# Optimization experiments

Measured on AMD Instinct MI355X. Metric: run time of the kernel, lower is better.

The kernel has to match this reference:

```python
import jax, jax.numpy as jnp
import numpy as np

B, N, C, H = 2, 2048, 1024, 16
HD = C // H
FF = 2 * C


def _layernorm(x, w, b, eps=1e-5):
    mu = jnp.mean(x, axis=-1, keepdims=True)
    var = jnp.var(x, axis=-1, keepdims=True)
    return (x - mu) * jax.lax.rsqrt(var + eps) * w + b


def setup_inputs() -> dict:
    key = jax.random.key(0)
    ks = jax.random.split(key, 16)
    std = 0.02
    d = {
        'q': jax.random.normal(ks[0], (B, N, C), jnp.float32),
        'k': jax.random.normal(ks[1], (B, N, C), jnp.float32),
        'v': jax.random.normal(ks[2], (B, N, C), jnp.float32),
        # attention projections (stored [in, out])
        'Wq': jax.random.normal(ks[3], (C, C), jnp.float32) * std,
        'bq': jnp.zeros((C,), jnp.float32),
        'Wk': jax.random.normal(ks[4], (C, C), jnp.float32) * std,
        'bk': jnp.zeros((C,), jnp.float32),
        'Wv': jax.random.normal(ks[5], (C, C), jnp.float32) * std,
        'bv': jnp.zeros((C,), jnp.float32),
        'Wo': jax.random.normal(ks[6], (C, C), jnp.float32) * std,
        'bo': jnp.zeros((C,), jnp.float32),
        # post-attention LayerNorm
        'ln_w': jnp.ones((C,), jnp.float32),
        'ln_b': jnp.zeros((C,), jnp.float32),
        # FFN
        'W1': jax.random.normal(ks[7], (C, FF), jnp.float32) * std,
        'b1': jnp.zeros((FF,), jnp.float32),
        'W2': jax.random.normal(ks[8], (FF, C), jnp.float32) * std,
        'b2': jnp.zeros((C,), jnp.float32),
    }
    return d


def reference(q, k, v, Wq, bq, Wk, bk, Wv, bv, Wo, bo, ln_w, ln_b, W1, b1, W2, b2):
    scale = HD ** -0.5
    # Note: the torch forward overwrites the normalized-input attention with
    # attention on raw q,k,v; only the second call affects the output.
    qh = (q @ Wq + bq).reshape(B, N, H, HD)  # [B,Nq,H,hd]
    kh = (k @ Wk + bk).reshape(B, N, H, HD)
    vh = (v @ Wv + bv).reshape(B, N, H, HD)
    attn = jnp.einsum('bqhd,bkhd->bhqk', qh, kh) * scale
    attn = jax.nn.softmax(attn, axis=-1)
    ctx = jnp.einsum('bhqk,bkhd->bqhd', attn, vh).reshape(B, N, C)
    x = ctx @ Wo + bo
    x = x + q  # residual (drop_path=0, dropout eval -> identity)
    h = _layernorm(x, ln_w, ln_b)
    y = jax.nn.gelu(h @ W1 + b1, approximate=False) @ W2 + b2
    return y + x
```

## Files before the change

kernel.cpp:

```cpp
#include <hip/hip_runtime.h>

constexpr int B_ = 2, N_ = 2048, C_ = 1024, H_ = 16, HD_ = 64, FF_ = 2048;

typedef __attribute__((ext_vector_type(8))) __bf16 bf16x8;
typedef __attribute__((ext_vector_type(4))) float f32x4;
typedef __attribute__((ext_vector_type(4))) short s16x4;

__device__ __forceinline__ unsigned short f2bf(float f) {
  union { float f; unsigned int u; } v; v.f = f;
  unsigned int r = v.u + 0x7fffu + ((v.u >> 16) & 1u);
  return (unsigned short)(r >> 16);
}

__device__ __forceinline__ void gload_lds16(const unsigned short* g, unsigned short* l) {
  __builtin_amdgcn_global_load_lds((const __attribute__((address_space(1))) void*)g,
                                   (__attribute__((address_space(3))) void*)l, 16, 0, 0);
}

__global__ __launch_bounds__(256)
void cast3_bf16(const float* __restrict__ q, const float* __restrict__ k,
                const float* __restrict__ v, unsigned short* __restrict__ qo,
                unsigned short* __restrict__ ko, unsigned short* __restrict__ vo, int n8) {
  int i = blockIdx.x * 256 + threadIdx.x;
  if (i >= n8) return;
  const float* in = blockIdx.z == 0 ? q : (blockIdx.z == 1 ? k : v);
  unsigned short* out = blockIdx.z == 0 ? qo : (blockIdx.z == 1 ? ko : vo);
  const float4 a = ((const float4*)in)[2 * i];
  const float4 b = ((const float4*)in)[2 * i + 1];
  uint4 o;
  o.x = (unsigned)f2bf(a.x) | ((unsigned)f2bf(a.y) << 16);
  o.y = (unsigned)f2bf(a.z) | ((unsigned)f2bf(a.w) << 16);
  o.z = (unsigned)f2bf(b.x) | ((unsigned)f2bf(b.y) << 16);
  o.w = (unsigned)f2bf(b.z) | ((unsigned)f2bf(b.w) << 16);
  ((uint4*)out)[i] = o;
}

__global__ __launch_bounds__(256)
void wt_cast(const float* __restrict__ W, unsigned short* __restrict__ Wt, int K, int N) {
  __shared__ unsigned short tile[32][33];
  const int tx = threadIdx.x, ty = threadIdx.y;
  const int n0 = blockIdx.x * 32, k0 = blockIdx.y * 32;
#pragma unroll
  for (int r = 0; r < 4; ++r)
    tile[ty + r * 8][tx] = f2bf(W[(size_t)(k0 + ty + r * 8) * N + n0 + tx]);
  __syncthreads();
#pragma unroll
  for (int r = 0; r < 4; ++r)
    Wt[(size_t)(n0 + ty + r * 8) * K + k0 + tx] = tile[tx][ty + r * 8];
}

__global__ __launch_bounds__(256)
void wt_cast4(const float* __restrict__ Wa, const float* __restrict__ Wb,
              const float* __restrict__ Wc, const float* __restrict__ Wd,
              unsigned short* __restrict__ Oa, unsigned short* __restrict__ Ob,
              unsigned short* __restrict__ Oc, unsigned short* __restrict__ Od) {
  __shared__ unsigned short tile[32][33];
  const int z = blockIdx.z;
  const float* W = z == 0 ? Wa : (z == 1 ? Wb : (z == 2 ? Wc : Wd));
  unsigned short* Wt = z == 0 ? Oa : (z == 1 ? Ob : (z == 2 ? Oc : Od));
  const int tx = threadIdx.x, ty = threadIdx.y;
  const int n0 = blockIdx.x * 32, k0 = blockIdx.y * 32;
#pragma unroll
  for (int r = 0; r < 4; ++r)
    tile[ty + r * 8][tx] = f2bf(W[(size_t)(k0 + ty + r * 8) * C_ + n0 + tx]);
  __syncthreads();
#pragma unroll
  for (int r = 0; r < 4; ++r)
    Wt[(size_t)(n0 + ty + r * 8) * C_ + k0 + tx] = tile[tx][ty + r * 8];
}

__global__ __launch_bounds__(256)
void vh_transpose(const unsigned short* __restrict__ Vh, unsigned short* __restrict__ VhT) {
  __shared__ unsigned short tile[32][33];
  const int tx = threadIdx.x, ty = threadIdx.y;
  const int bh = blockIdx.z, b = bh >> 4, h = bh & 15;
  const int n0 = blockIdx.x * 32, d0 = blockIdx.y * 32;
#pragma unroll
  for (int r = 0; r < 4; ++r) {
    int n = n0 + ty + r * 8;
    tile[ty + r * 8][tx] = Vh[((size_t)(b * N_ + n)) * C_ + h * HD_ + d0 + tx];
  }
  __syncthreads();
#pragma unroll
  for (int r = 0; r < 4; ++r) {
    int d = d0 + ty + r * 8;
    VhT[((size_t)(bh * HD_ + d)) * N_ + n0 + tx] = tile[tx][ty + r * 8];
  }
}

__global__ __launch_bounds__(256, 2)
void gemm_qkv(const unsigned short* __restrict__ A0, const unsigned short* __restrict__ A1,
              const unsigned short* __restrict__ A2, const unsigned short* __restrict__ B0,
              const unsigned short* __restrict__ B1, const unsigned short* __restrict__ B2,
              const float* __restrict__ c0, const float* __restrict__ c1v,
              const float* __restrict__ c2, unsigned short* __restrict__ O0,
              unsigned short* __restrict__ O1, unsigned short* __restrict__ O2) {
  const int z = blockIdx.z;
  const unsigned short* A = z == 0 ? A0 : (z == 1 ? A1 : A2);
  const unsigned short* Bt = z == 0 ? B0 : (z == 1 ? B1 : B2);
  const float* bias = z == 0 ? c0 : (z == 1 ? c1v : c2);
  unsigned short* outB = z == 0 ? O0 : (z == 1 ? O1 : O2);
  const int K = C_, Nn = C_;

  __shared__ unsigned short lA[128 * 64];
  __shared__ unsigned short lB[128 * 64];
  const int t = threadIdx.x;
  const int lane = t & 63;
  const int w = t >> 6;
  const int wm = w >> 1, wn = w & 1;
  const int l15 = lane & 15, g = lane >> 4;

  const unsigned short* Ab = A + (size_t)blockIdx.x * 128 * K;
  const unsigned short* Bb = Bt + (size_t)blockIdx.y * 128 * K;

  f32x4 acc[4][4] = {};

  for (int k0 = 0; k0 < K; k0 += 64) {
    __syncthreads();
#pragma unroll
    for (int i = 0; i < 4; ++i) {
      int id = i * 256 + t;
      gload_lds16(Ab + (size_t)(id >> 3) * K + k0 + (id & 7) * 8, &lA[id * 8]);
    }
#pragma unroll
    for (int i = 0; i < 4; ++i) {
      int id = i * 256 + t;
      gload_lds16(Bb + (size_t)(id >> 3) * K + k0 + (id & 7) * 8, &lB[id * 8]);
    }
    __syncthreads();
#pragma unroll
    for (int kk = 0; kk < 2; ++kk) {
      bf16x8 af[4], bfr[4];
#pragma unroll
      for (int mi = 0; mi < 4; ++mi)
        af[mi] = *(const bf16x8*)&lA[(wm * 64 + mi * 16 + l15) * 64 + kk * 32 + g * 8];
#pragma unroll
      for (int ni = 0; ni < 4; ++ni)
        bfr[ni] = *(const bf16x8*)&lB[(wn * 64 + ni * 16 + l15) * 64 + kk * 32 + g * 8];
#pragma unroll
      for (int mi = 0; mi < 4; ++mi)
#pragma unroll
        for (int ni = 0; ni < 4; ++ni)
          acc[mi][ni] = __builtin_amdgcn_mfma_f32_16x16x32_bf16(af[mi], bfr[ni], acc[mi][ni], 0, 0, 0);
    }
  }

#pragma unroll
  for (int mi = 0; mi < 4; ++mi)
#pragma unroll
    for (int ni = 0; ni < 4; ++ni) {
      const int col = blockIdx.y * 128 + wn * 64 + ni * 16 + l15;
      const float bcol = bias[col];
#pragma unroll
      for (int r = 0; r < 4; ++r) {
        const int row = blockIdx.x * 128 + wm * 64 + mi * 16 + g * 4 + r;
        outB[(size_t)row * Nn + col] = f2bf(acc[mi][ni][r] + bcol);
      }
    }
}

template <int EPI>
__global__ __launch_bounds__(256, 2)
void gemm_bt(const unsigned short* __restrict__ A, const unsigned short* __restrict__ Bt,
             const float* __restrict__ bias, const float* __restrict__ resid,
             float* __restrict__ outF, unsigned short* __restrict__ outB,
             int M, int N, int K) {
  __shared__ unsigned short lA[128 * 64];
  __shared__ unsigned short lB[128 * 64];
  const int t = threadIdx.x;
  const int lane = t & 63;
  const int w = t >> 6;
  const int wm = w >> 1, wn = w & 1;
  const int l15 = lane & 15, g = lane >> 4;

  const unsigned short* Ab = A + (size_t)blockIdx.x * 128 * K;
  const unsigned short* Bb = Bt + (size_t)blockIdx.y * 128 * K;

  f32x4 acc[4][4] = {};

  for (int k0 = 0; k0 < K; k0 += 64) {
    __syncthreads();
#pragma unroll
    for (int i = 0; i < 4; ++i) {
      int id = i * 256 + t;
      gload_lds16(Ab + (size_t)(id >> 3) * K + k0 + (id & 7) * 8, &lA[id * 8]);
    }
#pragma unroll
    for (int i = 0; i < 4; ++i) {
      int id = i * 256 + t;
      gload_lds16(Bb + (size_t)(id >> 3) * K + k0 + (id & 7) * 8, &lB[id * 8]);
    }
    __syncthreads();
#pragma unroll
    for (int kk = 0; kk < 2; ++kk) {
      bf16x8 af[4], bfr[4];
#pragma unroll
      for (int mi = 0; mi < 4; ++mi)
        af[mi] = *(const bf16x8*)&lA[(wm * 64 + mi * 16 + l15) * 64 + kk * 32 + g * 8];
#pragma unroll
      for (int ni = 0; ni < 4; ++ni)
        bfr[ni] = *(const bf16x8*)&lB[(wn * 64 + ni * 16 + l15) * 64 + kk * 32 + g * 8];
#pragma unroll
      for (int mi = 0; mi < 4; ++mi)
#pragma unroll
        for (int ni = 0; ni < 4; ++ni)
          acc[mi][ni] = __builtin_amdgcn_mfma_f32_16x16x32_bf16(af[mi], bfr[ni], acc[mi][ni], 0, 0, 0);
    }
  }

#pragma unroll
  for (int mi = 0; mi < 4; ++mi)
#pragma unroll
    for (int ni = 0; ni < 4; ++ni) {
      const int col = blockIdx.y * 128 + wn * 64 + ni * 16 + l15;
      const float bcol = bias[col];
#pragma unroll
      for (int r = 0; r < 4; ++r) {
        const int row = blockIdx.x * 128 + wm * 64 + mi * 16 + g * 4 + r;
        const size_t o = (size_t)row * N + col;
        float val = acc[mi][ni][r] + bcol;
        if (EPI == 0) {
          outB[o] = f2bf(val);
        } else if (EPI == 1) {
          outF[o] = val + resid[o];
        } else {
          float ge = 0.5f * val * (1.0f + erff(val * 0.70710678118654752f));
          outB[o] = f2bf(ge);
        }
      }
    }
}

__global__ __launch_bounds__(256, 2)
void gemm_n64(const unsigned short* __restrict__ A, const unsigned short* __restrict__ Bt,
              const float* __restrict__ bias, const float* __restrict__ resid,
              float* __restrict__ outF, int M, int N, int K) {
  __shared__ unsigned short lA[128 * 64];
  __shared__ unsigned short lB[64 * 64];
  const int t = threadIdx.x;
  const int lane = t & 63;
  const int w = t >> 6;
  const int wm = w >> 1, wn = w & 1;
  const int l15 = lane & 15, g = lane >> 4;

  const unsigned short* Ab = A + (size_t)blockIdx.x * 128 * K;
  const unsigned short* Bb = Bt + (size_t)blockIdx.y * 64 * K;

  f32x4 acc[4][2] = {};

  for (int k0 = 0; k0 < K; k0 += 64) {
    __syncthreads();
#pragma unroll
    for (int i = 0; i < 4; ++i) {
      int id = i * 256 + t;
      gload_lds16(Ab + (size_t)(id >> 3) * K + k0 + (id & 7) * 8, &lA[id * 8]);
    }
#pragma unroll
    for (int i = 0; i < 2; ++i) {
      int id = i * 256 + t;
      gload_lds16(Bb + (size_t)(id >> 3) * K + k0 + (id & 7) * 8, &lB[id * 8]);
    }
    __syncthreads();
#pragma unroll
    for (int kk = 0; kk < 2; ++kk) {
      bf16x8 af[4], bfr[2];
#pragma unroll
      for (int mi = 0; mi < 4; ++mi)
        af[mi] = *(const bf16x8*)&lA[(wm * 64 + mi * 16 + l15) * 64 + kk * 32 + g * 8];
#pragma unroll
      for (int ni = 0; ni < 2; ++ni)
        bfr[ni] = *(const bf16x8*)&lB[(wn * 32 + ni * 16 + l15) * 64 + kk * 32 + g * 8];
#pragma unroll
      for (int mi = 0; mi < 4; ++mi)
#pragma unroll
        for (int ni = 0; ni < 2; ++ni)
          acc[mi][ni] = __builtin_amdgcn_mfma_f32_16x16x32_bf16(af[mi], bfr[ni], acc[mi][ni], 0, 0, 0);
    }
  }

#pragma unroll
  for (int mi = 0; mi < 4; ++mi)
#pragma unroll
    for (int ni = 0; ni < 2; ++ni) {
      const int col = blockIdx.y * 64 + wn * 32 + ni * 16 + l15;
      const float bcol = bias[col];
#pragma unroll
      for (int r = 0; r < 4; ++r) {
        const int row = blockIdx.x * 128 + wm * 64 + mi * 16 + g * 4 + r;
        const size_t o = (size_t)row * N + col;
        outF[o] = acc[mi][ni][r] + bcol + resid[o];
      }
    }
}

__global__ __launch_bounds__(256, 2)
void attn_fwd(const unsigned short* __restrict__ Qh, const unsigned short* __restrict__ Kh,
              const unsigned short* __restrict__ VhT, unsigned short* __restrict__ ctx) {
  __shared__ unsigned short lK[2][64 * 64];
  __shared__ unsigned short lV[2][64 * 64];

  const int t = threadIdx.x, lane = t & 63, w = t >> 6;
  const int l15 = lane & 15, g = lane >> 4;
  const int bh = blockIdx.y, b = bh >> 4, h = bh & 15;
  const int qb0 = blockIdx.x * 128 + w * 32;

  const unsigned short* Qb = Qh + (size_t)b * N_ * C_ + h * HD_;
  const unsigned short* Kb = Kh + (size_t)b * N_ * C_ + h * HD_;
  const unsigned short* Vb = VhT + (size_t)bh * HD_ * N_;

  bf16x8 qf[2][2];
#pragma unroll
  for (int qi = 0; qi < 2; ++qi)
#pragma unroll
    for (int kk = 0; kk < 2; ++kk)
      qf[qi][kk] = *(const bf16x8*)(Qb + (size_t)(qb0 + qi * 16 + l15) * C_ + kk * 32 + g * 8);

  auto stageK = [&](int buf, int kb) {
#pragma unroll
    for (int i = 0; i < 2; ++i) {
      int o = (i * 256 + t) * 16;
      int r = o >> 7;
      int c = (o & 127) ^ ((r & 7) << 4);
      gload_lds16(Kb + (size_t)(kb + r) * C_ + (c >> 1), &lK[buf][o >> 1]);
    }
  };
  auto stageV = [&](int buf, int kb) {
#pragma unroll
    for (int i = 0; i < 2; ++i) {
      int o = (i * 256 + t) * 16;
      int r = o >> 7;
      int c = (o & 127) ^ ((r & 7) << 4);
      gload_lds16(Vb + (size_t)r * N_ + kb + (c >> 1), &lV[buf][o >> 1]);
    }
  };

  f32x4 od[4][2] = {};
  float mrun[2] = {-1e30f, -1e30f};
  float srun[2] = {0.f, 0.f};
  const float c1 = 0.18033688011112042f;
  const float DTHR = 8.0f / 0.18033688011112042f;

  stageK(0, 0);
  stageV(0, 0);
  __syncthreads();

  int cur = 0;
  for (int tile = 0; tile < N_ / 64; ++tile) {
    if (tile + 1 < N_ / 64) {
      stageK(cur ^ 1, (tile + 1) * 64);
      stageV(cur ^ 1, (tile + 1) * 64);
    }

    f32x4 st[4][2];
#pragma unroll
    for (int kf = 0; kf < 4; ++kf) {
      const int krow = kf * 16 + l15;
      const int sw = (krow & 7) << 4;
      const bf16x8 ka = *(const bf16x8*)&lK[cur][krow * 64 + ((( g * 16) ^ sw) >> 1)];
      const bf16x8 kc = *(const bf16x8*)&lK[cur][krow * 64 + (((64 + g * 16) ^ sw) >> 1)];
#pragma unroll
      for (int qi = 0; qi < 2; ++qi) {
        f32x4 z = {};
        z = __builtin_amdgcn_mfma_f32_16x16x32_bf16(ka, qf[qi][0], z, 0, 0, 0);
        z = __builtin_amdgcn_mfma_f32_16x16x32_bf16(kc, qf[qi][1], z, 0, 0, 0);
        st[kf][qi] = z;
      }
    }

    s16x4 pb[4][2];
#pragma unroll
    for (int qi = 0; qi < 2; ++qi) {
      float mx = st[0][qi][0];
#pragma unroll
      for (int r = 1; r < 4; ++r) mx = fmaxf(mx, st[0][qi][r]);
#pragma unroll
      for (int kf = 1; kf < 4; ++kf)
#pragma unroll
        for (int r = 0; r < 4; ++r) mx = fmaxf(mx, st[kf][qi][r]);
      mx = fmaxf(mx, __shfl_xor(mx, 16));
      mx = fmaxf(mx, __shfl_xor(mx, 32));
      if (__any(mx > mrun[qi] + DTHR)) {
        const float mn = fmaxf(mrun[qi], mx);
        const float sf = exp2f((mrun[qi] - mn) * c1);
        mrun[qi] = mn;
        srun[qi] *= sf;
#pragma unroll
        for (int di = 0; di < 4; ++di)
#pragma unroll
          for (int r = 0; r < 4; ++r) od[di][qi][r] *= sf;
      }
      const float mc = mrun[qi] * c1;
#pragma unroll
      for (int kf = 0; kf < 4; ++kf) {
        union { s16x4 v; __bf16 e[4]; } u;
#pragma unroll
        for (int r = 0; r < 4; ++r) {
          float pv = exp2f(st[kf][qi][r] * c1 - mc);
          srun[qi] += pv;
          u.e[r] = (__bf16)pv;
        }
        pb[kf][qi] = u.v;
      }
    }

#pragma unroll
    for (int di = 0; di < 4; ++di) {
      const int vrow = di * 16 + l15;
      const int sw = (vrow & 7) << 4;
#pragma unroll
      for (int kf = 0; kf < 4; ++kf) {
        const s16x4 vt = *(const s16x4*)&lV[cur][vrow * 64 + (((kf * 32 + g * 8) ^ sw) >> 1)];
#pragma unroll
        for (int qi = 0; qi < 2; ++qi)
          od[di][qi] = __builtin_amdgcn_mfma_f32_16x16x16bf16_1k(vt, pb[kf][qi], od[di][qi], 0, 0, 0);
      }
    }

    __syncthreads();
    cur ^= 1;
  }

#pragma unroll
  for (int qi = 0; qi < 2; ++qi) {
    float s = srun[qi];
    s += __shfl_xor(s, 16);
    s += __shfl_xor(s, 32);
    float rinv = 1.0f / s;
    const int q = qb0 + qi * 16 + l15;
#pragma unroll
    for (int di = 0; di < 4; ++di)
#pragma unroll
      for (int r = 0; r < 4; ++r) {
        int d = di * 16 + g * 4 + r;
        ctx[((size_t)(b * N_ + q)) * C_ + h * HD_ + d] = f2bf(od[di][qi][r] * rinv);
      }
  }
}

__global__ __launch_bounds__(256)
void ln_kernel(const float* __restrict__ x, const float* __restrict__ lw,
               const float* __restrict__ lb, unsigned short* __restrict__ h) {
  const int row = blockIdx.x;
  const int t = threadIdx.x;
  const float4 v = ((const float4*)(x + (size_t)row * C_))[t];
  float sum = v.x + v.y + v.z + v.w;
#pragma unroll
  for (int m = 1; m < 64; m <<= 1) sum += __shfl_xor(sum, m);
  __shared__ float red[8];
  if ((t & 63) == 0) red[t >> 6] = sum;
  __syncthreads();
  const float mu = (red[0] + red[1] + red[2] + red[3]) * (1.0f / C_);
  const float d0 = v.x - mu, d1 = v.y - mu, d2 = v.z - mu, d3 = v.w - mu;
  float sq = d0 * d0 + d1 * d1 + d2 * d2 + d3 * d3;
#pragma unroll
  for (int m = 1; m < 64; m <<= 1) sq += __shfl_xor(sq, m);
  if ((t & 63) == 0) red[4 + (t >> 6)] = sq;
  __syncthreads();
  const float var = (red[4] + red[5] + red[6] + red[7]) * (1.0f / C_);
  const float rstd = rsqrtf(var + 1e-5f);
  const float4 ww = ((const float4*)lw)[t];
  const float4 bb = ((const float4*)lb)[t];
  uint2 o;
  o.x = (unsigned)f2bf(d0 * rstd * ww.x + bb.x) | ((unsigned)f2bf(d1 * rstd * ww.y + bb.y) << 16);
  o.y = (unsigned)f2bf(d2 * rstd * ww.z + bb.z) | ((unsigned)f2bf(d3 * rstd * ww.w + bb.w) << 16);
  ((uint2*)(h + (size_t)row * C_))[t] = o;
}

extern "C" void kernel_launch(void* const* d_in, const int* in_sizes, int n_in,
                              void* d_out, int out_size, void* d_ws, size_t ws_size,
                              hipStream_t stream) {
  const float* q   = (const float*)d_in[0];
  const float* k   = (const float*)d_in[1];
  const float* v   = (const float*)d_in[2];
  const float* Wq  = (const float*)d_in[3];
  const float* bq  = (const float*)d_in[4];
  const float* Wk  = (const float*)d_in[5];
  const float* bk  = (const float*)d_in[6];
  const float* Wv  = (const float*)d_in[7];
  const float* bv  = (const float*)d_in[8];
  const float* Wo  = (const float*)d_in[9];
  const float* bo  = (const float*)d_in[10];
  const float* lnw = (const float*)d_in[11];
  const float* lnb = (const float*)d_in[12];
  const float* W1  = (const float*)d_in[13];
  const float* b1  = (const float*)d_in[14];
  const float* W2  = (const float*)d_in[15];
  const float* b2  = (const float*)d_in[16];
  float* out = (float*)d_out;

  char* ws = (char*)d_ws;
  const size_t MB = 1024 * 1024;
  if (ws_size < 120 * MB) return;
  unsigned short* qb   = (unsigned short*)(ws + 0 * MB);
  unsigned short* kb   = (unsigned short*)(ws + 8 * MB);
  unsigned short* vb   = (unsigned short*)(ws + 16 * MB);
  unsigned short* Wqt  = (unsigned short*)(ws + 24 * MB);
  unsigned short* Wkt  = (unsigned short*)(ws + 26 * MB);
  unsigned short* Wvt  = (unsigned short*)(ws + 28 * MB);
  unsigned short* Wot  = (unsigned short*)(ws + 30 * MB);
  unsigned short* W1t  = (unsigned short*)(ws + 32 * MB);
  unsigned short* W2t  = (unsigned short*)(ws + 36 * MB);
  unsigned short* Qh   = (unsigned short*)(ws + 40 * MB);
  unsigned short* Kh   = (unsigned short*)(ws + 48 * MB);
  unsigned short* Vh   = (unsigned short*)(ws + 56 * MB);
  unsigned short* VhT  = (unsigned short*)(ws + 64 * MB);
  unsigned short* ctx  = (unsigned short*)(ws + 72 * MB);
  float*          xf   = (float*)(ws + 80 * MB);
  unsigned short* hb   = (unsigned short*)(ws + 96 * MB);
  unsigned short* tbuf = (unsigned short*)(ws + 104 * MB);

  const int n8 = B_ * N_ * C_ / 8;
  cast3_bf16<<<dim3((n8 + 255) / 256, 1, 3), 256, 0, stream>>>(q, k, v, qb, kb, vb, n8);

  dim3 blk32(32, 8);
  wt_cast4<<<dim3(C_ / 32, C_ / 32, 4), blk32, 0, stream>>>(Wq, Wk, Wv, Wo, Wqt, Wkt, Wvt, Wot);
  wt_cast<<<dim3(FF_ / 32, C_ / 32), blk32, 0, stream>>>(W1, W1t, C_, FF_);
  wt_cast<<<dim3(C_ / 32, FF_ / 32), blk32, 0, stream>>>(W2, W2t, FF_, C_);

  gemm_qkv<<<dim3(B_ * N_ / 128, C_ / 128, 3), 256, 0, stream>>>(qb, kb, vb, Wqt, Wkt, Wvt,
                                                                 bq, bk, bv, Qh, Kh, Vh);

  vh_transpose<<<dim3(N_ / 32, HD_ / 32, B_ * H_), blk32, 0, stream>>>(Vh, VhT);
  attn_fwd<<<dim3(N_ / 128, B_ * H_), 256, 0, stream>>>(Qh, Kh, VhT, ctx);

  gemm_n64<<<dim3(B_ * N_ / 128, C_ / 64), 256, 0, stream>>>(ctx, Wot, bo, q, xf, B_ * N_, C_, C_);
  ln_kernel<<<dim3(B_ * N_), 256, 0, stream>>>(xf, lnw, lnb, hb);
  gemm_bt<2><<<dim3(B_ * N_ / 128, FF_ / 128), 256, 0, stream>>>(hb, W1t, b1, nullptr, nullptr, tbuf,
                                                                 B_ * N_, FF_, C_);
  gemm_n64<<<dim3(B_ * N_ / 128, C_ / 64), 256, 0, stream>>>(tbuf, W2t, b2, xf, out, B_ * N_, C_, FF_);
}
```

Baseline: 245.3 us.

## Split attention block into 8 waves of 16 queries with MFMA priority hints

The attention kernel now launches 512 threads per block, so each of 8 waves handles 16 query rows instead of 4 waves handling 32. This halves per-wave register state (accumulators, scores, softmax stats), and each thread issues one staging load per tile instead of two. The change also raises occupancy bounds, wraps MFMA sections in s_setprio, and packs the output stores into 8-byte writes. In exchange, each wave reuses a K/V tile fragment across fewer queries, adding LDS read traffic per MFMA, and more waves wait at each barrier.

```diff
diff --git a/kernel.cpp b/kernel.cpp
--- a/kernel.cpp
+++ b/kernel.cpp
@@ -293,7 +293,7 @@
     }
 }
 
-__global__ __launch_bounds__(256, 2)
+__global__ __launch_bounds__(512, 4)
 void attn_fwd(const unsigned short* __restrict__ Qh, const unsigned short* __restrict__ Kh,
               const unsigned short* __restrict__ VhT, unsigned short* __restrict__ ctx) {
   __shared__ unsigned short lK[2][64 * 64];
@@ -302,41 +302,33 @@
   const int t = threadIdx.x, lane = t & 63, w = t >> 6;
   const int l15 = lane & 15, g = lane >> 4;
   const int bh = blockIdx.y, b = bh >> 4, h = bh & 15;
-  const int qb0 = blockIdx.x * 128 + w * 32;
+  const int qb0 = blockIdx.x * 128 + w * 16;
 
   const unsigned short* Qb = Qh + (size_t)b * N_ * C_ + h * HD_;
   const unsigned short* Kb = Kh + (size_t)b * N_ * C_ + h * HD_;
   const unsigned short* Vb = VhT + (size_t)bh * HD_ * N_;
 
-  bf16x8 qf[2][2];
-#pragma unroll
-  for (int qi = 0; qi < 2; ++qi)
-#pragma unroll
-    for (int kk = 0; kk < 2; ++kk)
-      qf[qi][kk] = *(const bf16x8*)(Qb + (size_t)(qb0 + qi * 16 + l15) * C_ + kk * 32 + g * 8);
+  bf16x8 qf[2];
+#pragma unroll
+  for (int kk = 0; kk < 2; ++kk)
+    qf[kk] = *(const bf16x8*)(Qb + (size_t)(qb0 + l15) * C_ + kk * 32 + g * 8);
 
   auto stageK = [&](int buf, int kb) {
-#pragma unroll
-    for (int i = 0; i < 2; ++i) {
-      int o = (i * 256 + t) * 16;
-      int r = o >> 7;
-      int c = (o & 127) ^ ((r & 7) << 4);
-      gload_lds16(Kb + (size_t)(kb + r) * C_ + (c >> 1), &lK[buf][o >> 1]);
-    }
+    int o = t * 16;
+    int r = o >> 7;
+    int c = (o & 127) ^ ((r & 7) << 4);
+    gload_lds16(Kb + (size_t)(kb + r) * C_ + (c >> 1), &lK[buf][o >> 1]);
   };
   auto stageV = [&](int buf, int kb) {
-#pragma unroll
-    for (int i = 0; i < 2; ++i) {
-      int o = (i * 256 + t) * 16;
-      int r = o >> 7;
-      int c = (o & 127) ^ ((r & 7) << 4);
-      gload_lds16(Vb + (size_t)r * N_ + kb + (c >> 1), &lV[buf][o >> 1]);
-    }
+    int o = t * 16;
+    int r = o >> 7;
+    int c = (o & 127) ^ ((r & 7) << 4);
+    gload_lds16(Vb + (size_t)r * N_ + kb + (c >> 1), &lV[buf][o >> 1]);
   };
 
-  f32x4 od[4][2] = {};
-  float mrun[2] = {-1e30f, -1e30f};
-  float srun[2] = {0.f, 0.f};
+  f32x4 od[4] = {};
+  float mrun = -1e30f;
+  float srun = 0.f;
   const float c1 = 0.18033688011112042f;
   const float DTHR = 8.0f / 0.18033688011112042f;
 
@@ -351,58 +343,55 @@
       stageV(cur ^ 1, (tile + 1) * 64);
     }
 
-    f32x4 st[4][2];
+    f32x4 st[4];
+    __builtin_amdgcn_s_setprio(1);
 #pragma unroll
     for (int kf = 0; kf < 4; ++kf) {
       const int krow = kf * 16 + l15;
       const int sw = (krow & 7) << 4;
       const bf16x8 ka = *(const bf16x8*)&lK[cur][krow * 64 + ((( g * 16) ^ sw) >> 1)];
       const bf16x8 kc = *(const bf16x8*)&lK[cur][krow * 64 + (((64 + g * 16) ^ sw) >> 1)];
-#pragma unroll
-      for (int qi = 0; qi < 2; ++qi) {
-        f32x4 z = {};
-        z = __builtin_amdgcn_mfma_f32_16x16x32_bf16(ka, qf[qi][0], z, 0, 0, 0);
-        z = __builtin_amdgcn_mfma_f32_16x16x32_bf16(kc, qf[qi][1], z, 0, 0, 0);
-        st[kf][qi] = z;
+      f32x4 z = {};
+      z = __builtin_amdgcn_mfma_f32_16x16x32_bf16(ka, qf[0], z, 0, 0, 0);
+      z = __builtin_amdgcn_mfma_f32_16x16x32_bf16(kc, qf[1], z, 0, 0, 0);
+      st[kf] = z;
+    }
+    __builtin_amdgcn_s_setprio(0);
+
+    float mx = st[0][0];
+#pragma unroll
+    for (int r = 1; r < 4; ++r) mx = fmaxf(mx, st[0][r]);
+#pragma unroll
+    for (int kf = 1; kf < 4; ++kf)
+#pragma unroll
+      for (int r = 0; r < 4; ++r) mx = fmaxf(mx, st[kf][r]);
+    mx = fmaxf(mx, __shfl_xor(mx, 16));
+    mx = fmaxf(mx, __shfl_xor(mx, 32));
+    if (__any(mx > mrun + DTHR)) {
+      const float mn = fmaxf(mrun, mx);
+      const float sf = exp2f((mrun - mn) * c1);
+      mrun = mn;
+      srun *= sf;
+#pragma unroll
+      for (int di = 0; di < 4; ++di)
+#pragma unroll
+        for (int r = 0; r < 4; ++r) od[di][r] *= sf;
+    }
+    const float mc = mrun * c1;
+    s16x4 pb[4];
+#pragma unroll
+    for (int kf = 0; kf < 4; ++kf) {
+      union { s16x4 v; __bf16 e[4]; } u;
+#pragma unroll
+      for (int r = 0; r < 4; ++r) {
+        float pv = exp2f(st[kf][r] * c1 - mc);
+        srun += pv;
+        u.e[r] = (__bf16)pv;
       }
-    }
-
-    s16x4 pb[4][2];
-#pragma unroll
-    for (int qi = 0; qi < 2; ++qi) {
-      float mx = st[0][qi][0];
-#pragma unroll
-      for (int r = 1; r < 4; ++r) mx = fmaxf(mx, st[0][qi][r]);
-#pragma unroll
-      for (int kf = 1; kf < 4; ++kf)
-#pragma unroll
-        for (int r = 0; r < 4; ++r) mx = fmaxf(mx, st[kf][qi][r]);
-      mx = fmaxf(mx, __shfl_xor(mx, 16));
-      mx = fmaxf(mx, __shfl_xor(mx, 32));
-      if (__any(mx > mrun[qi] + DTHR)) {
-        const float mn = fmaxf(mrun[qi], mx);
-        const float sf = exp2f((mrun[qi] - mn) * c1);
-        mrun[qi] = mn;
-        srun[qi] *= sf;
-#pragma unroll
-        for (int di = 0; di < 4; ++di)
-#pragma unroll
-          for (int r = 0; r < 4; ++r) od[di][qi][r] *= sf;
-      }
-      const float mc = mrun[qi] * c1;
-#pragma unroll
-      for (int kf = 0; kf < 4; ++kf) {
-        union { s16x4 v; __bf16 e[4]; } u;
-#pragma unroll
-        for (int r = 0; r < 4; ++r) {
-          float pv = exp2f(st[kf][qi][r] * c1 - mc);
-          srun[qi] += pv;
-          u.e[r] = (__bf16)pv;
-        }
-        pb[kf][qi] = u.v;
-      }
-    }
-
+      pb[kf] = u.v;
+    }
+
+    __builtin_amdgcn_s_setprio(1);
 #pragma unroll
     for (int di = 0; di < 4; ++di) {
       const int vrow = di * 16 + l15;
@@ -410,30 +399,27 @@
 #pragma unroll
       for (int kf = 0; kf < 4; ++kf) {
         const s16x4 vt = *(const s16x4*)&lV[cur][vrow * 64 + (((kf * 32 + g * 8) ^ sw) >> 1)];
-#pragma unroll
-        for (int qi = 0; qi < 2; ++qi)
-          od[di][qi] = __builtin_amdgcn_mfma_f32_16x16x16bf16_1k(vt, pb[kf][qi], od[di][qi], 0, 0, 0);
+        od[di] = __builtin_amdgcn_mfma_f32_16x16x16bf16_1k(vt, pb[kf], od[di], 0, 0, 0);
       }
     }
+    __builtin_amdgcn_s_setprio(0);
 
     __syncthreads();
     cur ^= 1;
   }
 
-#pragma unroll
-  for (int qi = 0; qi < 2; ++qi) {
-    float s = srun[qi];
-    s += __shfl_xor(s, 16);
-    s += __shfl_xor(s, 32);
-    float rinv = 1.0f / s;
-    const int q = qb0 + qi * 16 + l15;
-#pragma unroll
-    for (int di = 0; di < 4; ++di)
-#pragma unroll
-      for (int r = 0; r < 4; ++r) {
-        int d = di * 16 + g * 4 + r;
-        ctx[((size_t)(b * N_ + q)) * C_ + h * HD_ + d] = f2bf(od[di][qi][r] * rinv);
-      }
+  float s = srun;
+  s += __shfl_xor(s, 16);
+  s += __shfl_xor(s, 32);
+  const float rinv = 1.0f / s;
+  const int q = qb0 + l15;
+  unsigned short* cp = ctx + ((size_t)(b * N_ + q)) * C_ + h * HD_;
+#pragma unroll
+  for (int di = 0; di < 4; ++di) {
+    uint2 o;
+    o.x = (unsigned)f2bf(od[di][0] * rinv) | ((unsigned)f2bf(od[di][1] * rinv) << 16);
+    o.y = (unsigned)f2bf(od[di][2] * rinv) | ((unsigned)f2bf(od[di][3] * rinv) << 16);
+    *(uint2*)(cp + di * 16 + g * 4) = o;
   }
 }
 
@@ -521,7 +507,7 @@
                                                                  bq, bk, bv, Qh, Kh, Vh);
 
   vh_transpose<<<dim3(N_ / 32, HD_ / 32, B_ * H_), blk32, 0, stream>>>(Vh, VhT);
-  attn_fwd<<<dim3(N_ / 128, B_ * H_), 256, 0, stream>>>(Qh, Kh, VhT, ctx);
+  attn_fwd<<<dim3(N_ / 128, B_ * H_), 512, 0, stream>>>(Qh, Kh, VhT, ctx);
 
   gemm_n64<<<dim3(B_ * N_ / 128, C_ / 64), 256, 0, stream>>>(ctx, Wot, bo, q, xf, B_ * N_, C_, C_);
   ln_kernel<<<dim3(B_ * N_), 256, 0, stream>>>(xf, lnw, lnb, hb);
```

New measurement: 241.8 us. Within noise of the previous version (-1.4%).
